# Performance work log

Hardware: AMD Instinct MI355X
Metric: run time of the kernel (lower is better)

The kernel has to match this reference:

```python
import jax, jax.numpy as jnp
import numpy as np

B, S, D_IN, D_OUT, H = 4, 2048, 1024, 1024, 16
HD = D_OUT // H

def setup_inputs() -> dict:
    key = jax.random.key(0)
    ks = jax.random.split(key, 6)
    s = 1.0 / np.sqrt(D_IN)
    return {
        "x": jax.random.normal(ks[0], (B, S, D_IN), dtype=jnp.float32),
        "Wq": jax.random.uniform(ks[1], (D_IN, D_OUT), jnp.float32, -s, s),
        "Wk": jax.random.uniform(ks[2], (D_IN, D_OUT), jnp.float32, -s, s),
        "Wv": jax.random.uniform(ks[3], (D_IN, D_OUT), jnp.float32, -s, s),
        "Wo": jax.random.uniform(ks[4], (D_OUT, D_OUT), jnp.float32, -s, s),
        "bo": jax.random.uniform(ks[5], (D_OUT,), jnp.float32, -s, s),
    }

def reference(x, Wq, Wk, Wv, Wo, bo):
    b, n, _ = x.shape
    # project and split heads: [b, h, n, hd]
    q = (x @ Wq).reshape(b, n, H, HD).transpose(0, 2, 1, 3)
    k = (x @ Wk).reshape(b, n, H, HD).transpose(0, 2, 1, 3)
    v = (x @ Wv).reshape(b, n, H, HD).transpose(0, 2, 1, 3)
    scores = jnp.einsum("bhqd,bhkd->bhqk", q, k) / np.sqrt(HD).astype(np.float32)
    causal = jnp.tril(jnp.ones((n, n), dtype=bool))
    scores = jnp.where(causal, scores, -jnp.inf)
    attn = jax.nn.softmax(scores, axis=-1)  # dropout p=0.0 -> identity
    ctx = jnp.einsum("bhqk,bhkd->bhqd", attn, v)
    ctx = ctx.transpose(0, 2, 1, 3).reshape(b, n, D_OUT)
    return ctx @ Wo + bo
```

## Files before the change

kernel.cpp:

```cpp
#include <hip/hip_runtime.h>
#include <stdint.h>

#define B_   4
#define S_   2048
#define DI   1024
#define DOUT 1024
#define NHD  16
#define HD   64

typedef __attribute__((ext_vector_type(8))) short short8;
typedef __attribute__((ext_vector_type(4))) float f32x4;
typedef __attribute__((ext_vector_type(16))) float f32x16;

__device__ __forceinline__ unsigned short f32_bf16(float f) {
  union { float f; unsigned u; } v; v.f = f;
  unsigned r = v.u + 0x7FFFu + ((v.u >> 16) & 1u);
  return (unsigned short)(r >> 16);
}

__device__ __forceinline__ unsigned cvt_pk_bf16(float a, float b) {
  unsigned r;
  asm("v_cvt_pk_bf16_f32 %0, %1, %2" : "=v"(r) : "v"(a), "v"(b));
  return r;
}

__device__ __forceinline__ void pl32swap(unsigned &dst, unsigned &src) {
  asm("v_permlane32_swap_b32 %0, %1" : "+v"(dst), "+v"(src));
}

__device__ __forceinline__ float max3f(float a, float b, float c) {
  float d;
  asm("v_max3_f32 %0, %1, %2, %3" : "=v"(d) : "v"(a), "v"(b), "v"(c));
  return d;
}

__device__ __forceinline__ void gl_lds16(const void* g, void* s) {
  __builtin_amdgcn_global_load_lds(
      (const __attribute__((address_space(1))) unsigned int*)g,
      (__attribute__((address_space(3))) unsigned int*)s, 16, 0, 0);
}

#define EXP2(x) __builtin_amdgcn_exp2f(x)

__global__ __launch_bounds__(256) void cvt_kernel(const float* __restrict__ src,
                                                  unsigned short* __restrict__ dst, int n4) {
  int i = blockIdx.x * blockDim.x + threadIdx.x;
  if (i < n4) {
    float4 v = ((const float4*)src)[i];
    ushort4 o;
    o.x = f32_bf16(v.x); o.y = f32_bf16(v.y); o.z = f32_bf16(v.z); o.w = f32_bf16(v.w);
    ((ushort4*)dst)[i] = o;
  }
}

__global__ __launch_bounds__(256) void wtrans_kernel(const float* __restrict__ W,
                                                     unsigned short* __restrict__ Wt) {
  __shared__ __attribute__((aligned(16))) float tile[64][65];
  const int k0 = blockIdx.y * 64;
  const int n0 = blockIdx.x * 64;
  const int tid = threadIdx.x;
#pragma unroll
  for (int i = 0; i < 4; i++) {
    int c = tid + i * 256;
    int r = c >> 4;
    int cc = (c & 15) * 4;
    float4 v = *(const float4*)(W + (size_t)(k0 + r) * DOUT + n0 + cc);
    tile[r][cc] = v.x; tile[r][cc + 1] = v.y; tile[r][cc + 2] = v.z; tile[r][cc + 3] = v.w;
  }
  __syncthreads();
#pragma unroll
  for (int i = 0; i < 4; i++) {
    int c = tid + i * 256;
    int r = c >> 4;
    int cc = (c & 15) * 4;
    ushort4 o;
    o.x = f32_bf16(tile[cc + 0][r]);
    o.y = f32_bf16(tile[cc + 1][r]);
    o.z = f32_bf16(tile[cc + 2][r]);
    o.w = f32_bf16(tile[cc + 3][r]);
    *(ushort4*)(Wt + (size_t)(n0 + r) * DI + k0 + cc) = o;
  }
}

__device__ __forceinline__ int cswz(int r, int c) {
  return r * 128 + ((((c >> 3) ^ ((r >> 3) & 15)) << 3) | (c & 7));
}

template <int MODE>
__global__ __launch_bounds__(256) void gemm_kernel(
    const unsigned short* __restrict__ A,
    const unsigned short* __restrict__ Bt,
    unsigned short* __restrict__ oQ,
    unsigned short* __restrict__ oK,
    unsigned short* __restrict__ oV,
    float* __restrict__ outF,
    const float* __restrict__ bias,
    int M, int N, int K) {
  __shared__ __attribute__((aligned(16))) unsigned short smem[MODE == 0 ? 16384 : 8192];
  unsigned short* Asm_ = smem;
  unsigned short* Bsm_ = smem + 4096;
  const int tid = threadIdx.x;
  const int lane = tid & 63;
  const int w = tid >> 6;
  const int wm = w >> 1, wn = w & 1;
  const int quad = lane >> 4, l16 = lane & 15;
  const int m0 = blockIdx.x * 128;
  const int n0 = blockIdx.y * 128;

  const int lr = lane >> 2;
  const int lc8 = (lane & 3) * 8;
  const unsigned short* gA0 = A + (size_t)(m0 + w * 32 + lr) * K + lc8;
  const unsigned short* gA1 = gA0 + (size_t)16 * K;
  const unsigned short* gB0 = Bt + (size_t)(n0 + w * 32 + lr) * K + lc8;
  const unsigned short* gB1 = gB0 + (size_t)16 * K;
  unsigned short* sA0 = Asm_ + (w * 2 + 0) * 512;
  unsigned short* sA1 = Asm_ + (w * 2 + 1) * 512;
  unsigned short* sB0 = Bsm_ + (w * 2 + 0) * 512;
  unsigned short* sB1 = Bsm_ + (w * 2 + 1) * 512;

  f32x4 acc[4][4] = {};

  for (int k0 = 0; k0 < K; k0 += 32) {
    __syncthreads();
    gl_lds16(gA0 + k0, sA0);
    gl_lds16(gA1 + k0, sA1);
    gl_lds16(gB0 + k0, sB0);
    gl_lds16(gB1 + k0, sB1);
    __syncthreads();
    short8 af[4], bfr[4];
#pragma unroll
    for (int mi = 0; mi < 4; mi++)
      af[mi] = *(const short8*)(Asm_ + (wm * 64 + mi * 16 + l16) * 32 + quad * 8);
#pragma unroll
    for (int ni = 0; ni < 4; ni++)
      bfr[ni] = *(const short8*)(Bsm_ + (wn * 64 + ni * 16 + l16) * 32 + quad * 8);
#pragma unroll
    for (int mi = 0; mi < 4; mi++)
#pragma unroll
      for (int ni = 0; ni < 4; ni++)
        acc[mi][ni] = __builtin_amdgcn_mfma_f32_16x16x32_bf16(af[mi], bfr[ni], acc[mi][ni], 0, 0, 0);
  }

  if (MODE == 0) {
    const int which = n0 >> 10;
    if (which == 2) {
      __syncthreads();
#pragma unroll
      for (int mi = 0; mi < 4; mi++)
#pragma unroll
        for (int ni = 0; ni < 4; ni++)
#pragma unroll
          for (int r = 0; r < 4; r++)
            smem[cswz(wm * 64 + mi * 16 + quad * 4 + r, wn * 64 + ni * 16 + l16)] =
                f32_bf16(acc[mi][ni][r]);
      __syncthreads();
      const int b = m0 >> 11, sb = m0 & 2047;
#pragma unroll
      for (int i = 0; i < 8; i++) {
        int c = tid + i * 256;
        int cl = c >> 4;
        int sc = (c & 15) * 8;
        int col = n0 + cl;
        int hh = (col >> 6) & 15, hd = col & 63;
        union { unsigned short u[8]; uint4 v; } t;
#pragma unroll
        for (int j = 0; j < 8; j++) t.u[j] = smem[cswz(sc + j, cl)];
        *(uint4*)(oV + (((size_t)(b * NHD + hh)) * HD + hd) * S_ + sb + sc) = t.v;
      }
    } else {
      unsigned short* dst0 = which == 0 ? oQ : oK;
#pragma unroll
      for (int mi = 0; mi < 4; mi++)
#pragma unroll
        for (int ni = 0; ni < 4; ni++) {
          const int col = n0 + wn * 64 + ni * 16 + l16;
          const int hh = (col >> 6) & 15, hd = col & 63;
#pragma unroll
          for (int r = 0; r < 4; r++) {
            const int row = m0 + wm * 64 + mi * 16 + quad * 4 + r;
            int b = row >> 11, s = row & 2047;
            dst0[(((size_t)(b * NHD + hh)) * S_ + s) * HD + hd] = f32_bf16(acc[mi][ni][r]);
          }
        }
    }
  } else {
#pragma unroll
    for (int mi = 0; mi < 4; mi++)
#pragma unroll
      for (int ni = 0; ni < 4; ni++) {
        const int col = n0 + wn * 64 + ni * 16 + l16;
        float bv = bias[col];
#pragma unroll
        for (int r = 0; r < 4; r++) {
          const int row = m0 + wm * 64 + mi * 16 + quad * 4 + r;
          outF[(size_t)row * N + col] = acc[mi][ni][r] + bv;
        }
      }
  }
}

__global__ __launch_bounds__(256, 2) void attn_kernel(
    const unsigned short* __restrict__ Q,
    const unsigned short* __restrict__ Kmat,
    const unsigned short* __restrict__ Vt,
    unsigned short* __restrict__ ctx) {
  __shared__ __attribute__((aligned(16))) unsigned short Ks[2][64 * 64];
  __shared__ __attribute__((aligned(16))) unsigned short Vs[2][64 * 64];
  __shared__ __attribute__((aligned(16))) unsigned short PsT[128 * 72];

  const int tid = threadIdx.x;
  const int lane = tid & 63;
  const int w = tid >> 6;
  const int l32 = lane & 31;
  const int h = lane >> 5;

  const int bh = blockIdx.x & 63;
  const int jj = blockIdx.x >> 6;

  const unsigned short* Qh = Q + (size_t)bh * S_ * HD;
  const unsigned short* Kh = Kmat + (size_t)bh * S_ * HD;
  const unsigned short* Vh = Vt + (size_t)bh * HD * S_;

  const int sr = tid >> 2;
  const int jA = tid & 3, jB = jA + 4;
  const int sswA = sr * 64 + ((jA ^ (sr & 7)) << 3);
  const int sswB = sr * 64 + ((jB ^ (sr & 7)) << 3);
  const unsigned short* gKA = Kh + (size_t)sr * HD + jA * 8;
  const unsigned short* gKB = Kh + (size_t)sr * HD + jB * 8;
  const unsigned short* gVA = Vh + (size_t)sr * S_ + jA * 8;
  const unsigned short* gVB = Vh + (size_t)sr * S_ + jB * 8;
  const int swz = (l32 & 7);

  unsigned short* myP = PsT + (size_t)(w * 32) * 72;
  const float scl = 0.18033688f;
  const int b = bh >> 4, head = bh & 15;

  for (int ph = 0; ph < 2; ph++) {
    const int qc = (ph == 0) ? (jj * 8 + w) : (63 - jj * 8 - w);
    const int nt = (qc >> 1) + 1;
    const int ntmax = (ph == 0) ? (jj * 4 + 2) : (32 - jj * 4);
    const int qrow = qc * 32 + l32;

    short8 qf[4];
#pragma unroll
    for (int ks = 0; ks < 4; ks++)
      qf[ks] = *(const short8*)(Qh + (size_t)qrow * HD + ks * 16 + h * 8);

    uint4 kregA = *(const uint4*)gKA, kregB = *(const uint4*)gKB;
    uint4 vregA = *(const uint4*)gVA, vregB = *(const uint4*)gVB;
    *(uint4*)(&Ks[0][sswA]) = kregA;
    *(uint4*)(&Ks[0][sswB]) = kregB;
    *(uint4*)(&Vs[0][sswA]) = vregA;
    *(uint4*)(&Vs[0][sswB]) = vregB;
    __syncthreads();

    f32x16 oacc[2] = {};
    float m_run = -__builtin_inff();
    float l_run = 0.f;

    for (int kt = 0; kt < ntmax; kt++) {
      if (kt + 1 < ntmax) {
        kregA = *(const uint4*)(gKA + (size_t)(kt + 1) * 64 * HD);
        kregB = *(const uint4*)(gKB + (size_t)(kt + 1) * 64 * HD);
        vregA = *(const uint4*)(gVA + (size_t)(kt + 1) * 64);
        vregB = *(const uint4*)(gVB + (size_t)(kt + 1) * 64);
      }
      const unsigned short* Kb_ = Ks[kt & 1];
      const unsigned short* Vb_ = Vs[kt & 1];

      if (kt < nt) {
        const int k0 = kt * 64;
        f32x16 sacc[2] = {};
#pragma unroll
        for (int ks = 0; ks < 4; ks++)
#pragma unroll
          for (int mi = 0; mi < 2; mi++) {
            short8 kf = *(const short8*)(Kb_ + (mi * 32 + l32) * 64 + (((ks * 2 + h) ^ swz) << 3));
            sacc[mi] = __builtin_amdgcn_mfma_f32_32x32x16_bf16(kf, qf[ks], sacc[mi], 0, 0, 0);
          }

        if (kt == nt - 1) {
#pragma unroll
          for (int mi = 0; mi < 2; mi++)
#pragma unroll
            for (int e = 0; e < 16; e++) {
              int key = k0 + mi * 32 + (e & 3) + 8 * (e >> 2) + 4 * h;
              if (key > qrow) sacc[mi][e] = -__builtin_inff();
            }
        }
        float vmax = fmaxf(sacc[0][0], sacc[0][1]);
#pragma unroll
        for (int e = 2; e < 16; e += 2) vmax = max3f(vmax, sacc[0][e], sacc[0][e + 1]);
#pragma unroll
        for (int e = 0; e < 16; e += 2) vmax = max3f(vmax, sacc[1][e], sacc[1][e + 1]);
        vmax = fmaxf(vmax, __shfl_xor(vmax, 32));
        const float pm = vmax * scl;
        if (!__all(pm <= m_run + 8.f)) {
          const float mnew = fmaxf(m_run, pm);
          const float alpha = EXP2(m_run - mnew);
          m_run = mnew;
          l_run *= alpha;
#pragma unroll
          for (int mi = 0; mi < 2; mi++) oacc[mi] *= alpha;
        }

        float rs = 0.f;
#pragma unroll
        for (int mi = 0; mi < 2; mi++)
#pragma unroll
          for (int e = 0; e < 16; e++) {
            float p = EXP2(fmaf(sacc[mi][e], scl, -m_run));
            sacc[mi][e] = p;
            rs += p;
          }
        rs += __shfl_xor(rs, 32);
        l_run += rs;

        short8 pfr[4];
#pragma unroll
        for (int mi = 0; mi < 2; mi++) {
          unsigned w0 = cvt_pk_bf16(sacc[mi][0], sacc[mi][1]);
          unsigned w1 = cvt_pk_bf16(sacc[mi][2], sacc[mi][3]);
          unsigned w2 = cvt_pk_bf16(sacc[mi][4], sacc[mi][5]);
          unsigned w3 = cvt_pk_bf16(sacc[mi][6], sacc[mi][7]);
          pl32swap(w0, w2);
          pl32swap(w1, w3);
          union { unsigned u[4]; short8 s; } lo;
          lo.u[0] = w0; lo.u[1] = w1; lo.u[2] = w2; lo.u[3] = w3;
          pfr[2 * mi + 0] = lo.s;
          unsigned x0 = cvt_pk_bf16(sacc[mi][8], sacc[mi][9]);
          unsigned x1 = cvt_pk_bf16(sacc[mi][10], sacc[mi][11]);
          unsigned x2 = cvt_pk_bf16(sacc[mi][12], sacc[mi][13]);
          unsigned x3 = cvt_pk_bf16(sacc[mi][14], sacc[mi][15]);
          pl32swap(x0, x2);
          pl32swap(x1, x3);
          union { unsigned u[4]; short8 s; } hi;
          hi.u[0] = x0; hi.u[1] = x1; hi.u[2] = x2; hi.u[3] = x3;
          pfr[2 * mi + 1] = hi.s;
        }

#pragma unroll
        for (int ks2 = 0; ks2 < 4; ks2++) {
#pragma unroll
          for (int mi2 = 0; mi2 < 2; mi2++) {
            short8 vf = *(const short8*)(Vb_ + (mi2 * 32 + l32) * 64 + (((ks2 * 2 + h) ^ swz) << 3));
            oacc[mi2] = __builtin_amdgcn_mfma_f32_32x32x16_bf16(vf, pfr[ks2], oacc[mi2], 0, 0, 0);
          }
        }
      }

      if (kt + 1 < ntmax) {
        *(uint4*)(&Ks[(kt + 1) & 1][sswA]) = kregA;
        *(uint4*)(&Ks[(kt + 1) & 1][sswB]) = kregB;
        *(uint4*)(&Vs[(kt + 1) & 1][sswA]) = vregA;
        *(uint4*)(&Vs[(kt + 1) & 1][sswB]) = vregB;
      }
      __syncthreads();
    }

    const float inv = 1.f / l_run;
#pragma unroll
    for (int mi2 = 0; mi2 < 2; mi2++)
#pragma unroll
      for (int g = 0; g < 4; g++) {
        uint2 pk;
        pk.x = cvt_pk_bf16(oacc[mi2][4 * g + 0] * inv, oacc[mi2][4 * g + 1] * inv);
        pk.y = cvt_pk_bf16(oacc[mi2][4 * g + 2] * inv, oacc[mi2][4 * g + 3] * inv);
        *(uint2*)(myP + l32 * 72 + mi2 * 32 + g * 8 + h * 4) = pk;
      }
#pragma unroll
    for (int p = 0; p < 4; p++) {
      int r = p * 8 + (lane >> 3);
      int c = (lane & 7) * 8;
      uint4 vv = *(const uint4*)(myP + r * 72 + c);
      *(uint4*)(ctx + ((size_t)(b * S_ + qc * 32 + r)) * DOUT + head * 64 + c) = vv;
    }
  }
}

extern "C" void kernel_launch(void* const* d_in, const int* in_sizes, int n_in,
                              void* d_out, int out_size, void* d_ws, size_t ws_size,
                              hipStream_t stream) {
  const float* x  = (const float*)d_in[0];
  const float* Wq = (const float*)d_in[1];
  const float* Wk = (const float*)d_in[2];
  const float* Wv = (const float*)d_in[3];
  const float* Wo = (const float*)d_in[4];
  const float* bo = (const float*)d_in[5];
  float* out = (float*)d_out;
  char* ws = (char*)d_ws;

  const size_t MB = 1024 * 1024;
  unsigned short* Wqt = (unsigned short*)(ws + 0 * MB);
  unsigned short* Wkt = (unsigned short*)(ws + 2 * MB);
  unsigned short* Wvt = (unsigned short*)(ws + 4 * MB);
  unsigned short* Wot = (unsigned short*)(ws + 6 * MB);
  unsigned short* xb  = (unsigned short*)(ws + 8 * MB);
  unsigned short* Qb  = (unsigned short*)(ws + 24 * MB);
  unsigned short* Kb  = (unsigned short*)(ws + 40 * MB);
  unsigned short* Vtb = (unsigned short*)(ws + 72 * MB);
  unsigned short* ctxb = xb;

  cvt_kernel<<<8192, 256, 0, stream>>>(x, xb, 2097152);
  wtrans_kernel<<<dim3(16, 16), 256, 0, stream>>>(Wq, Wqt);
  wtrans_kernel<<<dim3(16, 16), 256, 0, stream>>>(Wk, Wkt);
  wtrans_kernel<<<dim3(16, 16), 256, 0, stream>>>(Wv, Wvt);
  wtrans_kernel<<<dim3(16, 16), 256, 0, stream>>>(Wo, Wot);
  gemm_kernel<0><<<dim3(64, 24), 256, 0, stream>>>(xb, Wqt, Qb, Kb, Vtb, nullptr, nullptr,
                                                   8192, 3072, 1024);
  attn_kernel<<<512, 256, 0, stream>>>(Qb, Kb, Vtb, ctxb);
  gemm_kernel<1><<<dim3(64, 8), 256, 0, stream>>>(ctxb, Wot, nullptr, nullptr, nullptr, out, bo,
                                                  8192, 1024, 1024);
}
```

Baseline: 255.3 us.

## Double-buffer GEMM LDS tiles and merge four weight-transpose launches into one

The GEMM main loop now prefetches the next K-slice into a second LDS buffer with global_load_lds while computing on the current one, cutting the per-iteration barriers from two to one. This is meant to overlap global-memory latency with MFMA work. The four separate weight-transpose launches are folded into one launch with a z-dimension that selects the matrix, which saves launch overhead. The MODE 1 GEMM now uses 32KB of LDS instead of 16KB, which may reduce occupancy.

```diff
diff --git a/kernel.cpp b/kernel.cpp
--- a/kernel.cpp
+++ b/kernel.cpp
@@ -53,9 +53,15 @@
   }
 }
 
-__global__ __launch_bounds__(256) void wtrans_kernel(const float* __restrict__ W,
-                                                     unsigned short* __restrict__ Wt) {
+__global__ __launch_bounds__(256) void wtrans4_kernel(
+    const float* __restrict__ W0, const float* __restrict__ W1,
+    const float* __restrict__ W2, const float* __restrict__ W3,
+    unsigned short* __restrict__ T0, unsigned short* __restrict__ T1,
+    unsigned short* __restrict__ T2, unsigned short* __restrict__ T3) {
   __shared__ __attribute__((aligned(16))) float tile[64][65];
+  const int z = blockIdx.z;
+  const float* W = z == 0 ? W0 : z == 1 ? W1 : z == 2 ? W2 : W3;
+  unsigned short* Wt = z == 0 ? T0 : z == 1 ? T1 : z == 2 ? T2 : T3;
   const int k0 = blockIdx.y * 64;
   const int n0 = blockIdx.x * 64;
   const int tid = threadIdx.x;
@@ -96,9 +102,7 @@
     float* __restrict__ outF,
     const float* __restrict__ bias,
     int M, int N, int K) {
-  __shared__ __attribute__((aligned(16))) unsigned short smem[MODE == 0 ? 16384 : 8192];
-  unsigned short* Asm_ = smem;
-  unsigned short* Bsm_ = smem + 4096;
+  __shared__ __attribute__((aligned(16))) unsigned short smem[16384];
   const int tid = threadIdx.x;
   const int lane = tid & 63;
   const int w = tid >> 6;
@@ -113,38 +117,46 @@
   const unsigned short* gA1 = gA0 + (size_t)16 * K;
   const unsigned short* gB0 = Bt + (size_t)(n0 + w * 32 + lr) * K + lc8;
   const unsigned short* gB1 = gB0 + (size_t)16 * K;
-  unsigned short* sA0 = Asm_ + (w * 2 + 0) * 512;
-  unsigned short* sA1 = Asm_ + (w * 2 + 1) * 512;
-  unsigned short* sB0 = Bsm_ + (w * 2 + 0) * 512;
-  unsigned short* sB1 = Bsm_ + (w * 2 + 1) * 512;
+  const int sA0o = (w * 2 + 0) * 512;
+  const int sA1o = (w * 2 + 1) * 512;
+  const int sB0o = 4096 + (w * 2 + 0) * 512;
+  const int sB1o = 4096 + (w * 2 + 1) * 512;
 
   f32x4 acc[4][4] = {};
 
+  gl_lds16(gA0, smem + sA0o);
+  gl_lds16(gA1, smem + sA1o);
+  gl_lds16(gB0, smem + sB0o);
+  gl_lds16(gB1, smem + sB1o);
+  __syncthreads();
+
   for (int k0 = 0; k0 < K; k0 += 32) {
-    __syncthreads();
-    gl_lds16(gA0 + k0, sA0);
-    gl_lds16(gA1 + k0, sA1);
-    gl_lds16(gB0 + k0, sB0);
-    gl_lds16(gB1 + k0, sB1);
-    __syncthreads();
+    const int cb = ((k0 >> 5) & 1) << 13;
+    const int nb = 8192 - cb;
+    if (k0 + 32 < K) {
+      gl_lds16(gA0 + k0 + 32, smem + nb + sA0o);
+      gl_lds16(gA1 + k0 + 32, smem + nb + sA1o);
+      gl_lds16(gB0 + k0 + 32, smem + nb + sB0o);
+      gl_lds16(gB1 + k0 + 32, smem + nb + sB1o);
+    }
     short8 af[4], bfr[4];
 #pragma unroll
     for (int mi = 0; mi < 4; mi++)
-      af[mi] = *(const short8*)(Asm_ + (wm * 64 + mi * 16 + l16) * 32 + quad * 8);
+      af[mi] = *(const short8*)(smem + cb + (wm * 64 + mi * 16 + l16) * 32 + quad * 8);
 #pragma unroll
     for (int ni = 0; ni < 4; ni++)
-      bfr[ni] = *(const short8*)(Bsm_ + (wn * 64 + ni * 16 + l16) * 32 + quad * 8);
+      bfr[ni] = *(const short8*)(smem + cb + 4096 + (wn * 64 + ni * 16 + l16) * 32 + quad * 8);
 #pragma unroll
     for (int mi = 0; mi < 4; mi++)
 #pragma unroll
       for (int ni = 0; ni < 4; ni++)
         acc[mi][ni] = __builtin_amdgcn_mfma_f32_16x16x32_bf16(af[mi], bfr[ni], acc[mi][ni], 0, 0, 0);
+    __syncthreads();
   }
 
   if (MODE == 0) {
     const int which = n0 >> 10;
     if (which == 2) {
-      __syncthreads();
 #pragma unroll
       for (int mi = 0; mi < 4; mi++)
 #pragma unroll
@@ -402,10 +414,7 @@
   unsigned short* ctxb = xb;
 
   cvt_kernel<<<8192, 256, 0, stream>>>(x, xb, 2097152);
-  wtrans_kernel<<<dim3(16, 16), 256, 0, stream>>>(Wq, Wqt);
-  wtrans_kernel<<<dim3(16, 16), 256, 0, stream>>>(Wk, Wkt);
-  wtrans_kernel<<<dim3(16, 16), 256, 0, stream>>>(Wv, Wvt);
-  wtrans_kernel<<<dim3(16, 16), 256, 0, stream>>>(Wo, Wot);
+  wtrans4_kernel<<<dim3(16, 16, 4), 256, 0, stream>>>(Wq, Wk, Wv, Wo, Wqt, Wkt, Wvt, Wot);
   gemm_kernel<0><<<dim3(64, 24), 256, 0, stream>>>(xb, Wqt, Qb, Kb, Vtb, nullptr, nullptr,
                                                    8192, 3072, 1024);
   attn_kernel<<<512, 256, 0, stream>>>(Qb, Kb, Vtb, ctxb);
```

Measured after the change: 238.9 us. -6.4%, faster.
